# Performance work log

Measured on AMD Instinct MI355X. Metric: run time of the kernel, lower is better.

Reference implementation:

```python
import jax, jax.numpy as jnp
import numpy as np

SEASONP = 24
HORIZON = 12
F_WINDOW = 512
N_WINDOWS = 32768


def setup_inputs() -> dict:
    key = jax.random.key(0)
    k1, k2, k3, k4 = jax.random.split(key, 4)
    x = jax.random.uniform(k1, (N_WINDOWS, F_WINDOW), dtype=jnp.float32)
    y = jax.random.uniform(k2, (N_WINDOWS,), dtype=jnp.float32)
    init_L = jax.random.uniform(k3, (N_WINDOWS,), dtype=jnp.float32)
    init_b = jnp.zeros((N_WINDOWS,), dtype=jnp.float32)
    init_S = jax.random.uniform(k4, (N_WINDOWS, SEASONP), dtype=jnp.float32)
    return {
        "x": x,
        "y": y,
        "init_L": init_L,
        "init_b": init_b,
        "init_S": init_S,
        "alpha": jnp.float32(0.3),
        "beta": jnp.float32(0.1),
        "gamma": jnp.float32(0.2),
    }


def reference(x, y, init_L, init_b, init_S, alpha, beta, gamma):
    # Holt-Winters additive-seasonal recurrence, vectorized over N windows.
    # x: [N, F], init_L/init_b: [N], init_S: [N, P]
    N, F = x.shape
    P = init_S.shape[1]
    xt = x.T  # [F, N] time-major for scan
    idxs = jnp.arange(1, F, dtype=jnp.int32)

    def step(carry, inp):
        L, b, S = carry
        xi, i = inp
        si = i % P
        Sv = S[:, si]  # seasonal component for this phase, [N]
        Ln = alpha * (xi - Sv) + (1.0 - alpha) * (L + b)
        bn = beta * (Ln - L) + (1.0 - beta) * b
        Sn = S.at[:, si].set(gamma * (xi - Ln) + (1.0 - gamma) * Sv)
        return (Ln, bn, Sn), None

    (L, b, S), _ = jax.lax.scan(step, (init_L, init_b, init_S), (xt[1:], idxs))

    # forecast: f = (L[-1] + horizon * b[-1]) * S[(i + horizon) % P], i = F-1
    s_idx = (F - 1 + HORIZON) % P
    f = (L + HORIZON * b) * S[:, s_idx]
    loss = jnp.sum((f - y) ** 2)
    return loss
```

## Files before the change

### kernel.cpp

```cpp
#include <hip/hip_runtime.h>


#define F_WINDOW 512
#define SEASONP  24
#define HORIZON  12

#define HW_STEP(xi, si) do {                       \
    const float Sv  = S[si];                       \
    const float d   = (xi) - Sv;                   \
    const float ad  = alpha * d;         \
    const float s_  = L + b;                       \
    const float Ln  = fmaf(oma, s_, ad);           \
    const float abd = beta * ad;         \
    const float tb  = fmaf(omab, b, abd);          \
    const float bn  = fmaf(ab, -L, tb);            \
    const float e   = (xi) - Ln;                   \
    const float gs  = omg * Sv;                    \
    S[si] = fmaf(gamma, e, gs);                    \
    L = Ln; b = bn;                                \
} while (0)

#define HW_BLOCK24(v0, v1, v2, v3, v4, v5) do {                                  \
    HW_STEP(v0.x,  4); HW_STEP(v0.y,  5); HW_STEP(v0.z,  6); HW_STEP(v0.w,  7); \
    HW_STEP(v1.x,  8); HW_STEP(v1.y,  9); HW_STEP(v1.z, 10); HW_STEP(v1.w, 11); \
    HW_STEP(v2.x, 12); HW_STEP(v2.y, 13); HW_STEP(v2.z, 14); HW_STEP(v2.w, 15); \
    HW_STEP(v3.x, 16); HW_STEP(v3.y, 17); HW_STEP(v3.z, 18); HW_STEP(v3.w, 19); \
    HW_STEP(v4.x, 20); HW_STEP(v4.y, 21); HW_STEP(v4.z, 22); HW_STEP(v4.w, 23); \
    HW_STEP(v5.x,  0); HW_STEP(v5.y,  1); HW_STEP(v5.z,  2); HW_STEP(v5.w,  3); \
} while (0)

#define LOAD6(Bn, base) do {                                \
    Bn##0 = *(const float4*)((base) +  0);                  \
    Bn##1 = *(const float4*)((base) +  4);                  \
    Bn##2 = *(const float4*)((base) +  8);                  \
    Bn##3 = *(const float4*)((base) + 12);                  \
    Bn##4 = *(const float4*)((base) + 16);                  \
    Bn##5 = *(const float4*)((base) + 20);                  \
} while (0)

__global__ __launch_bounds__(64) void holtwinter_kernel(
    const float* __restrict__ x,
    const float* __restrict__ y,
    const float* __restrict__ init_L,
    const float* __restrict__ init_b,
    const float* __restrict__ init_S,
    const float* __restrict__ p_alpha,
    const float* __restrict__ p_beta,
    const float* __restrict__ p_gamma,
    float* __restrict__ out)
{
    const int n = blockIdx.x * 64 + threadIdx.x;

    const float alpha = p_alpha[0];
    const float beta  = p_beta[0];
    const float gamma = p_gamma[0];
    const float oma   = 1.0f - alpha;
    const float ab    = alpha * beta;
    const float omab  = 1.0f - ab;
    const float omg   = 1.0f - gamma;

    const float* __restrict__ xr = x + (size_t)n * F_WINDOW;

    float4 A0, A1, A2, A3, A4, A5;
    float4 B0, B1, B2, B3, B4, B5;
    float4 C0, C1, C2, C3, C4, C5;

    LOAD6(A, xr + 4);
    LOAD6(B, xr + 4 + 24);
    const float4 P = *(const float4*)(xr);
    const float4 T = *(const float4*)(xr + 508);
    const float  yv = y[n];
    const float  L0 = init_L[n];
    const float  b0 = init_b[n];

    float S[SEASONP];
    {
        const float4* iS4 = (const float4*)(init_S + (size_t)n * SEASONP);
        float4 s0 = iS4[0], s1 = iS4[1], s2 = iS4[2];
        float4 s3 = iS4[3], s4 = iS4[4], s5 = iS4[5];
        S[0]=s0.x;  S[1]=s0.y;  S[2]=s0.z;  S[3]=s0.w;
        S[4]=s1.x;  S[5]=s1.y;  S[6]=s1.z;  S[7]=s1.w;
        S[8]=s2.x;  S[9]=s2.y;  S[10]=s2.z; S[11]=s2.w;
        S[12]=s3.x; S[13]=s3.y; S[14]=s3.z; S[15]=s3.w;
        S[16]=s4.x; S[17]=s4.y; S[18]=s4.z; S[19]=s4.w;
        S[20]=s5.x; S[21]=s5.y; S[22]=s5.z; S[23]=s5.w;
    }

    float L = L0;
    float b = b0;

    HW_STEP(P.y, 1);
    HW_STEP(P.z, 2);
    HW_STEP(P.w, 3);

    #pragma unroll 1
    for (int k = 0; k < 6; ++k) {
        const float* base = xr + 4 + 72 * k;
        LOAD6(C, base + 48);
        HW_BLOCK24(A0, A1, A2, A3, A4, A5);
        LOAD6(A, base + 72);
        HW_BLOCK24(B0, B1, B2, B3, B4, B5);
        LOAD6(B, base + 96);
        HW_BLOCK24(C0, C1, C2, C3, C4, C5);
    }
    LOAD6(C, xr + 4 + 24 * 20);
    HW_BLOCK24(A0, A1, A2, A3, A4, A5);
    HW_BLOCK24(B0, B1, B2, B3, B4, B5);
    HW_BLOCK24(C0, C1, C2, C3, C4, C5);

    HW_STEP(T.x, 4); HW_STEP(T.y, 5); HW_STEP(T.z, 6); HW_STEP(T.w, 7);

    const float f    = fmaf((float)HORIZON, b, L) * S[19];
    const float diff = f - yv;
    float val = diff * diff;

    #pragma unroll
    for (int off = 32; off > 0; off >>= 1)
        val += __shfl_down(val, off);
    if (threadIdx.x == 0)
        atomicAdd(out, val);
}

extern "C" void kernel_launch(void* const* d_in, const int* in_sizes, int n_in,
                              void* d_out, int out_size, void* d_ws, size_t ws_size,
                              hipStream_t stream) {
    const float* x      = (const float*)d_in[0];
    const float* y      = (const float*)d_in[1];
    const float* init_L = (const float*)d_in[2];
    const float* init_b = (const float*)d_in[3];
    const float* init_S = (const float*)d_in[4];
    const float* alpha  = (const float*)d_in[5];
    const float* beta   = (const float*)d_in[6];
    const float* gamma  = (const float*)d_in[7];
    float* out = (float*)d_out;

    const int N = in_sizes[1];

    hipMemsetAsync(d_out, 0, (size_t)out_size * sizeof(float), stream);
    holtwinter_kernel<<<N / 64, 64, 0, stream>>>(
        x, y, init_L, init_b, init_S, alpha, beta, gamma, out);
}
```

Measured before the change: 121.5 us.

## Stage coalesced x loads through double-buffered LDS for per-thread recurrence

Before, each thread read its own 2 KB row with strided float4 loads. Now the 64 threads of a block load 96-element slabs cooperatively, so consecutive threads hit consecutive addresses. Each slab is written to a padded, double-buffered LDS tile and each thread then reads its own row from LDS, with the next slab's global loads issued before the current compute. Scheduling barriers pin the load/compute order. The change aims to cut uncoalesced global traffic, at the cost of about 51 KB of LDS per 64-thread block (lower occupancy), 96 staging registers, and block-wide syncs.

```diff
diff --git a/kernel.cpp b/kernel.cpp
--- a/kernel.cpp
+++ b/kernel.cpp
@@ -4,14 +4,17 @@
 #define F_WINDOW 512
 #define SEASONP  24
 #define HORIZON  12
+#define LSTRIDE  100
+
+#define SBAR() __builtin_amdgcn_sched_barrier(0)
 
 #define HW_STEP(xi, si) do {                       \
     const float Sv  = S[si];                       \
     const float d   = (xi) - Sv;                   \
-    const float ad  = alpha * d;         \
+    const float ad  = alpha * d;                   \
     const float s_  = L + b;                       \
     const float Ln  = fmaf(oma, s_, ad);           \
-    const float abd = beta * ad;         \
+    const float abd = beta * ad;                   \
     const float tb  = fmaf(omab, b, abd);          \
     const float bn  = fmaf(ab, -L, tb);            \
     const float e   = (xi) - Ln;                   \
@@ -29,13 +32,31 @@
     HW_STEP(v5.x,  0); HW_STEP(v5.y,  1); HW_STEP(v5.z,  2); HW_STEP(v5.w,  3); \
 } while (0)
 
-#define LOAD6(Bn, base) do {                                \
-    Bn##0 = *(const float4*)((base) +  0);                  \
-    Bn##1 = *(const float4*)((base) +  4);                  \
-    Bn##2 = *(const float4*)((base) +  8);                  \
-    Bn##3 = *(const float4*)((base) + 12);                  \
-    Bn##4 = *(const float4*)((base) + 16);                  \
-    Bn##5 = *(const float4*)((base) + 20);                  \
+#define ISSUE_LOADS(sb) do {                                      \
+    const float* gp = xblk + 4 + 96 * (sb);                       \
+    int r = r0, c = c0;                                           \
+    _Pragma("unroll")                                             \
+    for (int j = 0; j < 24; ++j) {                                \
+        stg[j] = *(const float4*)(gp + r * F_WINDOW + 4 * c);     \
+        c += 16; r += 2;                                          \
+        if (c >= 24) { c -= 24; r += 1; }                         \
+    }                                                             \
+} while (0)
+
+#define WRITE_LDS(buf) do {                                       \
+    int r = r0, c = c0;                                           \
+    _Pragma("unroll")                                             \
+    for (int j = 0; j < 24; ++j) {                                \
+        *(float4*)((buf) + r * LSTRIDE + 4 * c) = stg[j];         \
+        c += 16; r += 2;                                          \
+        if (c >= 24) { c -= 24; r += 1; }                         \
+    }                                                             \
+} while (0)
+
+#define READ6(Bn, k) do {                                         \
+    Bn##0 = rowp[6*(k)+0]; Bn##1 = rowp[6*(k)+1];                 \
+    Bn##2 = rowp[6*(k)+2]; Bn##3 = rowp[6*(k)+3];                 \
+    Bn##4 = rowp[6*(k)+4]; Bn##5 = rowp[6*(k)+5];                 \
 } while (0)
 
 __global__ __launch_bounds__(64) void holtwinter_kernel(
@@ -49,7 +70,12 @@
     const float* __restrict__ p_gamma,
     float* __restrict__ out)
 {
-    const int n = blockIdx.x * 64 + threadIdx.x;
+    __shared__ float lds[2][64 * LSTRIDE];
+
+    const int t = threadIdx.x;
+    const int n = blockIdx.x * 64 + t;
+    const int r0 = t / 24;
+    const int c0 = t - r0 * 24;
 
     const float alpha = p_alpha[0];
     const float beta  = p_beta[0];
@@ -59,20 +85,14 @@
     const float omab  = 1.0f - ab;
     const float omg   = 1.0f - gamma;
 
-    const float* __restrict__ xr = x + (size_t)n * F_WINDOW;
+    const float* __restrict__ xblk = x + (size_t)blockIdx.x * 64 * F_WINDOW;
+    const float* __restrict__ xr   = x + (size_t)n * F_WINDOW;
 
-    float4 A0, A1, A2, A3, A4, A5;
-    float4 B0, B1, B2, B3, B4, B5;
-    float4 C0, C1, C2, C3, C4, C5;
-
-    LOAD6(A, xr + 4);
-    LOAD6(B, xr + 4 + 24);
-    const float4 P = *(const float4*)(xr);
-    const float4 T = *(const float4*)(xr + 508);
+    const float4 P  = *(const float4*)(xr);
+    const float4 T  = *(const float4*)(xr + 508);
     const float  yv = y[n];
     const float  L0 = init_L[n];
     const float  b0 = init_b[n];
-
     float S[SEASONP];
     {
         const float4* iS4 = (const float4*)(init_S + (size_t)n * SEASONP);
@@ -86,29 +106,65 @@
         S[20]=s5.x; S[21]=s5.y; S[22]=s5.z; S[23]=s5.w;
     }
 
+    float4 stg[24];
+    float* bcur = lds[0];
+    float* bnxt = lds[1];
+
+    ISSUE_LOADS(0);
+    SBAR();
+
     float L = L0;
     float b = b0;
 
     HW_STEP(P.y, 1);
     HW_STEP(P.z, 2);
     HW_STEP(P.w, 3);
+    SBAR();
+
+    WRITE_LDS(bcur);
+    __syncthreads();
+
+    float4 R0, R1, R2, R3, R4, R5;
+    float4 Q0, Q1, Q2, Q3, Q4, Q5;
 
     #pragma unroll 1
-    for (int k = 0; k < 6; ++k) {
-        const float* base = xr + 4 + 72 * k;
-        LOAD6(C, base + 48);
-        HW_BLOCK24(A0, A1, A2, A3, A4, A5);
-        LOAD6(A, base + 72);
-        HW_BLOCK24(B0, B1, B2, B3, B4, B5);
-        LOAD6(B, base + 96);
-        HW_BLOCK24(C0, C1, C2, C3, C4, C5);
+    for (int s = 0; s < 4; ++s) {
+        ISSUE_LOADS(s + 1); SBAR();
+        const float4* rowp = (const float4*)(bcur + t * LSTRIDE);
+        READ6(R, 0); READ6(Q, 1); SBAR();
+        HW_BLOCK24(R0, R1, R2, R3, R4, R5); SBAR();
+        READ6(R, 2); SBAR();
+        HW_BLOCK24(Q0, Q1, Q2, Q3, Q4, Q5); SBAR();
+        READ6(Q, 3); SBAR();
+        HW_BLOCK24(R0, R1, R2, R3, R4, R5); SBAR();
+        HW_BLOCK24(Q0, Q1, Q2, Q3, Q4, Q5); SBAR();
+        WRITE_LDS(bnxt); SBAR();
+        __syncthreads();
+        float* tmp = bcur; bcur = bnxt; bnxt = tmp;
     }
-    LOAD6(C, xr + 4 + 24 * 20);
-    HW_BLOCK24(A0, A1, A2, A3, A4, A5);
-    HW_BLOCK24(B0, B1, B2, B3, B4, B5);
-    HW_BLOCK24(C0, C1, C2, C3, C4, C5);
 
-    HW_STEP(T.x, 4); HW_STEP(T.y, 5); HW_STEP(T.z, 6); HW_STEP(T.w, 7);
+    {
+        const float4* rowp = (const float4*)(bcur + t * LSTRIDE);
+        READ6(R, 0); READ6(Q, 1); SBAR();
+        HW_BLOCK24(R0, R1, R2, R3, R4, R5); SBAR();
+        READ6(R, 2); SBAR();
+        HW_BLOCK24(Q0, Q1, Q2, Q3, Q4, Q5); SBAR();
+        READ6(Q, 3); SBAR();
+        HW_BLOCK24(R0, R1, R2, R3, R4, R5); SBAR();
+        HW_BLOCK24(Q0, Q1, Q2, Q3, Q4, Q5);
+    }
+
+    {
+        const float4 v0 = *(const float4*)(xr + 484);
+        const float4 v1 = *(const float4*)(xr + 488);
+        const float4 v2 = *(const float4*)(xr + 492);
+        const float4 v3 = *(const float4*)(xr + 496);
+        const float4 v4 = *(const float4*)(xr + 500);
+        const float4 v5 = *(const float4*)(xr + 504);
+        HW_BLOCK24(v0, v1, v2, v3, v4, v5);
+        HW_STEP(T.x, 4); HW_STEP(T.y, 5);
+        HW_STEP(T.z, 6); HW_STEP(T.w, 7);
+    }
 
     const float f    = fmaf((float)HORIZON, b, L) * S[19];
     const float diff = f - yv;
@@ -117,7 +173,7 @@
     #pragma unroll
     for (int off = 32; off > 0; off >>= 1)
         val += __shfl_down(val, off);
-    if (threadIdx.x == 0)
+    if (t == 0)
         atomicAdd(out, val);
 }
 
```

Result: slower. 152.4 us (+25.4%).
